# Performance work log

Hardware: AMD Instinct MI355X
Metric: run time of the kernel (lower is better)

Reference implementation:

```python
import jax, jax.numpy as jnp
import numpy as np

# MANO prior contact vertex indices (f1+f2+f3+f4+f5+f0 from CMap_loss3)
_F1 = [697,698,699,700,712,713,714,715,737,738,739,740,741,743,744,745,746,748,749,750,753,754,755,756,757,758,759,760,761,762,763,764,765,766,767,768]
_F2 = [46,47,48,49,164,165,166,167,194,195,223,237,238,280,281,298,301,317,320,323,324,325,326,327,328,329,330,331,332,333,340,341,342,343,344,345,346,347,348,349,350,351,352,353,354,355]
_F3 = [356,357,358,359,375,376,386,387,396,397,402,403,413,429,433,434,435,436,437,438,439,440,441,442,443,444,452,453,454,455,456,459,460,461,462,463,464,465,466,467]
_F4 = [468,469,470,471,484,485,486,496,497,506,507,513,514,524,545,546,547,548,549,550,551,552,553,555,563,564,565,566,567,570,572,573,574,575,576,577,578]
_F5 = [580,581,582,583,600,601,602,614,615,624,625,630,631,641,663,664,665,666,667,668,670,672,680,681,682,683,684,686,687,688,689,690,691,692,693,694,695]
_F0 = [73,96,98,99,772,774,775,777]
PRIOR_IDX = np.array(_F1 + _F2 + _F3 + _F4 + _F5 + _F0, dtype=np.int32)


def _sqdist(a, b):
    # a: [B,N,3], b: [B,M,3] -> squared distances [B,N,M] via ||a||^2+||b||^2-2ab
    a2 = jnp.sum(a * a, -1)          # [B,N]
    b2 = jnp.sum(b * b, -1)          # [B,M]
    ab = jnp.einsum('bnd,bmd->bnm', a, b)
    return jnp.maximum(a2[:, :, None] + b2[:, None, :] - 2.0 * ab, 0.0)


def _knn1(src, trg):
    # nearest neighbor (K=1): squared dists + indices, like pytorch3d knn_points
    d2 = _sqdist(src, trg)           # [B,N,M]
    return jnp.min(d2, -1), jnp.argmin(d2, -1)


def _verts_normals(verts, faces):
    # area-weighted vertex normals (pytorch3d verts_normals_packed)
    v0 = verts[:, faces[:, 0]]       # [B,F,3]
    v1 = verts[:, faces[:, 1]]
    v2 = verts[:, faces[:, 2]]
    fn = jnp.cross(v1 - v0, v2 - v0)
    vn = jnp.zeros_like(verts)
    vn = vn.at[:, faces[:, 0]].add(fn).at[:, faces[:, 1]].add(fn).at[:, faces[:, 2]].add(fn)
    return vn / (jnp.linalg.norm(vn, axis=-1, keepdims=True) + 1e-12)


def setup_inputs() -> dict:
    key = jax.random.key(0)
    ks = jax.random.split(key, 8)
    B, N1, V, F, Z, P = 64, 8192, 778, 1538, 64, 61
    scale = 0.1  # keep points in a 0.1 box so contact thresholds (0.005/0.01) fire
    return {
        'obj_xyz': jax.random.uniform(ks[0], (B, N1, 3), jnp.float32) * scale,
        'recon_xyz': jax.random.uniform(ks[1], (B, V, 3), jnp.float32) * scale,
        'gt_xyz': jax.random.uniform(ks[2], (B, V, 3), jnp.float32) * scale,
        'mean': jax.random.normal(ks[3], (B, Z), jnp.float32),
        'log_var': jax.random.normal(ks[4], (B, Z), jnp.float32),
        'recon_param': jax.random.normal(ks[5], (B, P), jnp.float32),
        'x_param': jax.random.normal(ks[6], (B, P), jnp.float32),
        'faces': jax.random.randint(ks[7], (F, 3), 0, V, jnp.int32),
    }


def reference(obj_xyz, recon_xyz, gt_xyz, mean, log_var, recon_param, x_param, faces):
    B = obj_xyz.shape[0]
    fB = jnp.float32(B)

    # KNN from object points to gt / reconstructed hand (squared dists)
    d_gt, _ = _knn1(obj_xyz, gt_xyz)            # [B,N1]
    d_rec, idx_rec = _knn1(obj_xyz, recon_xyz)  # [B,N1], [B,N1]

    # param loss: MSE sum / B
    param_loss = jnp.sum((recon_param - x_param) ** 2) / fB

    # CVAE loss: chamfer (point_reduction='sum', batch_reduction='mean') + KLD
    d2 = _sqdist(recon_xyz, gt_xyz)             # [B,778,778]
    recon_loss = jnp.mean(jnp.sum(jnp.min(d2, -1), -1)) + jnp.mean(jnp.sum(jnp.min(d2, -2), -1))
    KLD = -0.5 * jnp.sum(1.0 + log_var - mean ** 2 - jnp.exp(log_var)) / fB * 10.0
    cvae_loss = recon_loss + KLD

    # CMap_loss3: obj NN distance to prior hand contact verts, masked by cmap
    cmap = d_rec < 0.01 ** 2                    # [B,N1] bool
    prior = recon_xyz[:, PRIOR_IDX, :]          # [B,222,3]
    obj_CD, _ = _knn1(obj_xyz, prior)           # [B,N1]
    n_points = jnp.sum(cmap).astype(jnp.float32)
    cmap_loss = 3000.0 * jnp.sum(jnp.where(cmap, obj_CD, 0.0)) / (fB * n_points)

    # CMap consistency: contact-map overlap ratio
    recon_cmap = jnp.sqrt(d_rec) < 0.005
    gt_cmap = jnp.sqrt(d_gt) < 0.005
    gt_cnum = jnp.sum(gt_cmap).astype(jnp.float32) + 0.0001
    consistency_loss = -5.0 * jnp.sum(recon_cmap & gt_cmap).astype(jnp.float32) / gt_cnum

    # inter-penetration: gather NN hand verts/normals, sign of dot, masked dist sum
    vn = _verts_normals(recon_xyz, faces)                               # [B,778,3]
    nn_v = jnp.take_along_axis(recon_xyz, idx_rec[..., None], axis=1)   # [B,N1,3]
    nn_n = jnp.take_along_axis(vn, idx_rec[..., None], axis=1)          # [B,N1,3]
    interior = jnp.sum((nn_v - obj_xyz) * nn_n, -1) > 0                 # [B,N1]
    penetr_loss = 100.0 * jnp.sum(jnp.where(interior, d_rec, 0.0)) / fB

    a, b, c, d, e = 1.0, 0.1, 1000.0, 10.0, 10.0
    loss = a * cvae_loss + b * param_loss + c * cmap_loss + d * consistency_loss + e * penetr_loss
    return loss
```

## Files before the change

### kernel.cpp

```cpp
#include <hip/hip_runtime.h>
#include <math.h>

#define NB     64
#define N1V    8192
#define NPTS   (NB * N1V)
#define NV     778
#define NVP    780
#define NQ     195
#define SEG1Q  51
#define NFACE  1538
#define NZ     64
#define NPAR   61
#define NPRIOR 204
#define PPT    8
#define BIAS   0.0625f

#define REC_BLOCKS 256
#define GT_BLOCKS  256
#define CH_BLOCKS  128
#define NROLE_BLOCKS (REC_BLOCKS + GT_BLOCKS + CH_BLOCKS)
#define CMB_BLOCKS 64

#define BATCH_F4 2352
#define ACC_OFF (NB * BATCH_F4 * 4)
#define RC_OFF  (ACC_OFF + 16)
#define GC_OFF  (RC_OFF + NPTS / 32)

__device__ __constant__ int c_prior[NPRIOR] = {
  697,698,699,700,712,713,714,715,737,738,739,740,741,743,744,745,746,748,749,750,
  753,754,755,756,757,758,759,760,761,762,763,764,765,766,767,768,
  46,47,48,49,164,165,166,167,194,195,223,237,238,280,281,298,301,317,320,323,
  324,325,326,327,328,329,330,331,332,333,340,341,342,343,344,345,346,347,348,349,
  350,351,352,353,354,355,
  356,357,358,359,375,376,386,387,396,397,402,403,413,429,433,434,435,436,437,438,
  439,440,441,442,443,444,452,453,454,455,456,459,460,461,462,463,464,465,466,467,
  468,469,470,471,484,485,486,496,497,506,507,513,514,524,545,546,547,548,549,550,
  551,552,553,555,563,564,565,566,567,570,572,573,574,575,576,577,578,
  580,581,582,583,600,601,602,614,615,624,625,630,631,641,663,664,665,666,667,668,
  670,672,680,681,682,683,684,686,687,688,689,690,691,692,693,694,695,
  73,96,98,99,772,774,775,777
};

__global__ __launch_bounds__(256) void k_prep(const float* __restrict__ recon,
                                              const float* __restrict__ gt,
                                              const int* __restrict__ faces,
                                              float4* __restrict__ ws4,
                                              float* __restrict__ acc) {
    int b = blockIdx.x, tid = threadIdx.x;
    if (b == 0 && tid < 16) acc[tid] = 0.0f;
    __shared__ float4 s_r[NV];
    __shared__ float s_vnx[NV], s_vny[NV], s_vnz[NV];
    __shared__ unsigned int s_bm[25];
    __shared__ unsigned short s_pre[26];
    __shared__ unsigned short s_perm[NV];

    if (tid < 25) s_bm[tid] = 0u;
    __syncthreads();
    if (tid < NPRIOR) {
        int v = c_prior[tid];
        atomicOr(&s_bm[v >> 5], 1u << (v & 31));
    }
    const float* rb = recon + (size_t)b * NV * 3;
    const float* gb = gt    + (size_t)b * NV * 3;
    float4* gt4   = ws4 + (size_t)b * BATCH_F4;
    float4* rec4p = gt4 + NVP;
    float4* nrm4p = rec4p + NVP;
    for (int j = tid; j < NV; j += 256) {
        float x = rb[3*j], y = rb[3*j+1], z = rb[3*j+2];
        s_r[j] = make_float4(x, y, z, x*x + y*y + z*z + BIAS);
        x = gb[3*j]; y = gb[3*j+1]; z = gb[3*j+2];
        gt4[j] = make_float4(x, y, z, x*x + y*y + z*z);
        s_vnx[j] = 0.0f; s_vny[j] = 0.0f; s_vnz[j] = 0.0f;
    }
    if (tid < 2) gt4[NV + tid] = make_float4(0.f, 0.f, 0.f, 1e30f);
    __syncthreads();
    if (tid == 0) {
        unsigned int run = 0;
        for (int w = 0; w < 25; ++w) { s_pre[w] = (unsigned short)run; run += __popc(s_bm[w]); }
        s_pre[25] = (unsigned short)run;
    }
    __syncthreads();
    for (int j = tid; j < NV; j += 256) {
        int w = j >> 5;
        unsigned int below = s_bm[w] & ((1u << (j & 31)) - 1u);
        int rank = s_pre[w] + __popc(below);
        bool member = (s_bm[w] >> (j & 31)) & 1u;
        int pos = member ? rank : (NPRIOR + (j - rank));
        s_perm[pos] = (unsigned short)j;
    }
    for (int f = tid; f < NFACE; f += 256) {
        int i0 = faces[3*f], i1 = faces[3*f+1], i2 = faces[3*f+2];
        float4 p0 = s_r[i0], p1 = s_r[i1], p2 = s_r[i2];
        float e1x = p1.x - p0.x, e1y = p1.y - p0.y, e1z = p1.z - p0.z;
        float e2x = p2.x - p0.x, e2y = p2.y - p0.y, e2z = p2.z - p0.z;
        float fx = e1y * e2z - e1z * e2y;
        float fy = e1z * e2x - e1x * e2z;
        float fz = e1x * e2y - e1y * e2x;
        atomicAdd(&s_vnx[i0], fx); atomicAdd(&s_vny[i0], fy); atomicAdd(&s_vnz[i0], fz);
        atomicAdd(&s_vnx[i1], fx); atomicAdd(&s_vny[i1], fy); atomicAdd(&s_vnz[i1], fz);
        atomicAdd(&s_vnx[i2], fx); atomicAdd(&s_vny[i2], fy); atomicAdd(&s_vnz[i2], fz);
    }
    __syncthreads();
    for (int j = tid; j < NVP; j += 256) {
        if (j < NV) {
            int src = s_perm[j];
            rec4p[j] = s_r[src];
            float x = s_vnx[src], y = s_vny[src], z = s_vnz[src];
            float inv = 1.0f / (sqrtf(x*x + y*y + z*z) + 1e-12f);
            nrm4p[j] = make_float4(x * inv, y * inv, z * inv, 0.0f);
        } else {
            rec4p[j] = make_float4(0.f, 0.f, 0.f, 1e30f);
            nrm4p[j] = make_float4(0.f, 0.f, 1.f, 0.0f);
        }
    }
}

#define LOAD_PTS(ob)                                                          \
    const float4* ob4 = (const float4*)((ob) + (size_t)tid * 24);             \
    float4 q0 = ob4[0], q1 = ob4[1], q2 = ob4[2],                             \
           q3 = ob4[3], q4 = ob4[4], q5 = ob4[5];                             \
    float px[PPT], py[PPT], pz[PPT];                                          \
    px[0]=q0.x; py[0]=q0.y; pz[0]=q0.z;  px[1]=q0.w; py[1]=q1.x; pz[1]=q1.y;  \
    px[2]=q1.z; py[2]=q1.w; pz[2]=q2.x;  px[3]=q2.y; py[3]=q2.z; pz[3]=q2.w;  \
    px[4]=q3.x; py[4]=q3.y; pz[4]=q3.z;  px[5]=q3.w; py[5]=q4.x; pz[5]=q4.y;  \
    px[6]=q4.z; py[6]=q4.w; pz[6]=q5.x;  px[7]=q5.y; py[7]=q5.z; pz[7]=q5.w;

__global__ __launch_bounds__(256) void k_fused(const float* __restrict__ obj,
                                               const float4* __restrict__ ws4,
                                               float* __restrict__ acc,
                                               unsigned char* __restrict__ rcA,
                                               unsigned char* __restrict__ gcA) {
    __shared__ float4 s_t[NVP];
    __shared__ float s_red[3];
    int tid = threadIdx.x;
    int blk = blockIdx.x;

    if (blk < REC_BLOCKS) {
        int b = blk >> 2, chunk = blk & 3;
        const float4* base = ws4 + (size_t)b * BATCH_F4;
        const float4* rec4p = base + NVP;
        const float4* nrm4p = base + 2 * NVP;
        for (int j = tid; j < NVP; j += 256) s_t[j] = rec4p[j];
        if (tid < 3) s_red[tid] = 0.0f;
        __syncthreads();

        const float* ob = obj + ((size_t)b * N1V + (size_t)chunk * 2048) * 3;
        LOAD_PTS(ob)
        float nax[PPT], nay[PPT], naz[PPT], m[PPT];
        int q[PPT];
#pragma unroll
        for (int i = 0; i < PPT; ++i) {
            nax[i] = -2.0f * px[i]; nay[i] = -2.0f * py[i]; naz[i] = -2.0f * pz[i];
            m[i] = 3.4e38f; q[i] = 0;
        }
        float mp[PPT];
#pragma unroll 1
        for (int jq = 0; jq < SEG1Q; ++jq) {
            int j = 4 * jq;
            float4 t0 = s_t[j], t1 = s_t[j+1], t2 = s_t[j+2], t3 = s_t[j+3];
#pragma unroll
            for (int i = 0; i < PPT; ++i) {
                float d0 = fmaf(nax[i], t0.x, fmaf(nay[i], t0.y, fmaf(naz[i], t0.z, t0.w)));
                float d1 = fmaf(nax[i], t1.x, fmaf(nay[i], t1.y, fmaf(naz[i], t1.z, t1.w)));
                float d2 = fmaf(nax[i], t2.x, fmaf(nay[i], t2.y, fmaf(naz[i], t2.z, t2.w)));
                float d3 = fmaf(nax[i], t3.x, fmaf(nay[i], t3.y, fmaf(naz[i], t3.z, t3.w)));
                float mn = fminf(fminf(fminf(d0, d1), fminf(d2, d3)), m[i]);
                q[i] = (mn < m[i]) ? jq : q[i];
                m[i] = mn;
            }
        }
#pragma unroll
        for (int i = 0; i < PPT; ++i) mp[i] = m[i];
#pragma unroll 1
        for (int jq = SEG1Q; jq < NQ; ++jq) {
            int j = 4 * jq;
            float4 t0 = s_t[j], t1 = s_t[j+1], t2 = s_t[j+2], t3 = s_t[j+3];
#pragma unroll
            for (int i = 0; i < PPT; ++i) {
                float d0 = fmaf(nax[i], t0.x, fmaf(nay[i], t0.y, fmaf(naz[i], t0.z, t0.w)));
                float d1 = fmaf(nax[i], t1.x, fmaf(nay[i], t1.y, fmaf(naz[i], t1.z, t1.w)));
                float d2 = fmaf(nax[i], t2.x, fmaf(nay[i], t2.y, fmaf(naz[i], t2.z, t2.w)));
                float d3 = fmaf(nax[i], t3.x, fmaf(nay[i], t3.y, fmaf(naz[i], t3.z, t3.w)));
                float mn = fminf(fminf(fminf(d0, d1), fminf(d2, d3)), m[i]);
                q[i] = (mn < m[i]) ? jq : q[i];
                m[i] = mn;
            }
        }
        float lS_cmap = 0.0f, lN_cmap = 0.0f, lS_pen = 0.0f;
        unsigned int rcbits = 0;
#pragma unroll
        for (int i = 0; i < PPT; ++i) {
            float a2 = px[i]*px[i] + py[i]*py[i] + pz[i]*pz[i];
            float drec = fmaxf(a2 + (m[i]  - BIAS), 0.0f);
            float dpri = fmaxf(a2 + (mp[i] - BIAS), 0.0f);
            bool cm = drec < 1e-4f;
            bool rc = sqrtf(drec) < 0.005f;
            if (cm) { lS_cmap += dpri; lN_cmap += 1.0f; }
            if (rc) rcbits |= (1u << i);
            int jr = 4 * q[i];
            float4 t0 = s_t[jr], t1 = s_t[jr+1], t2 = s_t[jr+2], t3 = s_t[jr+3];
            float d0 = fmaf(nax[i], t0.x, fmaf(nay[i], t0.y, fmaf(naz[i], t0.z, t0.w)));
            float d1 = fmaf(nax[i], t1.x, fmaf(nay[i], t1.y, fmaf(naz[i], t1.z, t1.w)));
            float d2 = fmaf(nax[i], t2.x, fmaf(nay[i], t2.y, fmaf(naz[i], t2.z, t2.w)));
            float d3 = fmaf(nax[i], t3.x, fmaf(nay[i], t3.y, fmaf(naz[i], t3.z, t3.w)));
            float mmin = fminf(fminf(d0, d1), fminf(d2, d3));
            int off = (d0 == mmin) ? 0 : ((d1 == mmin) ? 1 : ((d2 == mmin) ? 2 : 3));
            int jstar = jr + off;
            float4 tS = s_t[jstar];
            float4 nr = nrm4p[jstar];
            float ddot = (tS.x - px[i]) * nr.x + (tS.y - py[i]) * nr.y
                       + (tS.z - pz[i]) * nr.z;
            if (ddot > 0.0f) lS_pen += drec;
        }
        rcA[(size_t)blk * 256 + tid] = (unsigned char)rcbits;
        atomicAdd(&s_red[0], lS_cmap);
        atomicAdd(&s_red[1], lN_cmap);
        atomicAdd(&s_red[2], lS_pen);
        __syncthreads();
        if (tid == 0) atomicAdd(&acc[3], s_red[0]);
        if (tid == 1) atomicAdd(&acc[4], s_red[1]);
        if (tid == 2) atomicAdd(&acc[7], s_red[2]);
        return;
    }

    if (blk < REC_BLOCKS + GT_BLOCKS) {
        int r = blk - REC_BLOCKS;
        int b = r >> 2, chunk = r & 3;
        const float4* gt4v = ws4 + (size_t)b * BATCH_F4;
        for (int j = tid; j < NVP; j += 256) s_t[j] = gt4v[j];
        if (tid == 0) s_red[0] = 0.0f;
        __syncthreads();

        const float* ob = obj + ((size_t)b * N1V + (size_t)chunk * 2048) * 3;
        LOAD_PTS(ob)
        float nax[PPT], nay[PPT], naz[PPT], mgt[PPT];
#pragma unroll
        for (int i = 0; i < PPT; ++i) {
            nax[i] = -2.0f * px[i]; nay[i] = -2.0f * py[i]; naz[i] = -2.0f * pz[i];
            mgt[i] = 3.4e38f;
        }
#pragma unroll 1
        for (int jq = 0; jq < NQ; ++jq) {
            int j = 4 * jq;
            float4 t0 = s_t[j], t1 = s_t[j+1], t2 = s_t[j+2], t3 = s_t[j+3];
#pragma unroll
            for (int i = 0; i < PPT; ++i) {
                float d0 = fmaf(nax[i], t0.x, fmaf(nay[i], t0.y, fmaf(naz[i], t0.z, t0.w)));
                float d1 = fmaf(nax[i], t1.x, fmaf(nay[i], t1.y, fmaf(naz[i], t1.z, t1.w)));
                float d2 = fmaf(nax[i], t2.x, fmaf(nay[i], t2.y, fmaf(naz[i], t2.z, t2.w)));
                float d3 = fmaf(nax[i], t3.x, fmaf(nay[i], t3.y, fmaf(naz[i], t3.z, t3.w)));
                mgt[i] = fminf(fminf(mgt[i], fminf(d0, d1)), fminf(d2, d3));
            }
        }
        float lN_gt = 0.0f;
        unsigned int gcbits = 0;
#pragma unroll
        for (int i = 0; i < PPT; ++i) {
            float a2 = px[i]*px[i] + py[i]*py[i] + pz[i]*pz[i];
            float dgt = fmaxf(a2 + mgt[i], 0.0f);
            if (sqrtf(dgt) < 0.005f) { lN_gt += 1.0f; gcbits |= (1u << i); }
        }
        gcA[(size_t)r * 256 + tid] = (unsigned char)gcbits;
        atomicAdd(&s_red[0], lN_gt);
        __syncthreads();
        if (tid == 0) atomicAdd(&acc[5], s_red[0]);
        return;
    }

    {
        int c   = blk - (REC_BLOCKS + GT_BLOCKS);
        int b   = c >> 1;
        int dir = c & 1;
        const float4* base = ws4 + (size_t)b * BATCH_F4;
        const float4* srcv = dir ? base : (base + NVP);
        const float4* tgtv = dir ? (base + NVP) : base;
        for (int j = tid; j < NVP; j += 256) s_t[j] = tgtv[j];
        if (tid == 0) s_red[0] = 0.0f;
        __syncthreads();

        const int CPT = 4;
        float nax[CPT], nay[CPT], naz[CPT], a2[CPT], m[CPT];
        bool valid[CPT];
#pragma unroll
        for (int k = 0; k < CPT; ++k) {
            int p = tid + 256 * k;
            valid[k] = (p < NV);
            float4 s = srcv[valid[k] ? p : 0];
            nax[k] = -2.0f * s.x; nay[k] = -2.0f * s.y; naz[k] = -2.0f * s.z;
            a2[k] = s.w;
            m[k] = 3.4e38f;
        }
#pragma unroll 1
        for (int j = 0; j < NVP; j += 4) {
            float4 t0 = s_t[j], t1 = s_t[j+1], t2 = s_t[j+2], t3 = s_t[j+3];
#pragma unroll
            for (int k = 0; k < CPT; ++k) {
                float d0 = fmaf(nax[k], t0.x, fmaf(nay[k], t0.y, fmaf(naz[k], t0.z, t0.w)));
                float d1 = fmaf(nax[k], t1.x, fmaf(nay[k], t1.y, fmaf(naz[k], t1.z, t1.w)));
                float d2 = fmaf(nax[k], t2.x, fmaf(nay[k], t2.y, fmaf(naz[k], t2.z, t2.w)));
                float d3 = fmaf(nax[k], t3.x, fmaf(nay[k], t3.y, fmaf(naz[k], t3.z, t3.w)));
                m[k] = fminf(fminf(m[k], fminf(d0, d1)), fminf(d2, d3));
            }
        }
        float local = 0.0f;
#pragma unroll
        for (int k = 0; k < CPT; ++k)
            if (valid[k]) local += fmaxf(a2[k] + m[k] - BIAS, 0.0f);
        atomicAdd(&s_red[0], local);
        __syncthreads();
        if (tid == 0) atomicAdd(&acc[2], s_red[0]);
    }
}

__global__ __launch_bounds__(256) void k_combine(float* __restrict__ acc,
                                                 const unsigned int* __restrict__ rcW,
                                                 const unsigned int* __restrict__ gcW,
                                                 const float* __restrict__ mean,
                                                 const float* __restrict__ log_var,
                                                 const float* __restrict__ rp,
                                                 const float* __restrict__ xp,
                                                 float* __restrict__ out) {
    int blk = blockIdx.x, tid = threadIdx.x;
    __shared__ float s_red[2];
    __shared__ unsigned int s_ticket;
    if (tid < 2) s_red[tid] = 0.0f;
    __syncthreads();
    int idx = blk * 256 + tid;
    unsigned int rc = rcW[idx], gc = gcW[idx];
    float cnt = (float)__popc(rc & gc);
    atomicAdd(&s_red[0], cnt);
    __syncthreads();
    if (tid == 0) atomicAdd(&acc[6], s_red[0]);
    __threadfence();
    if (tid == 0) s_ticket = atomicAdd((unsigned int*)&acc[15], 1u);
    __syncthreads();

    if (s_ticket == CMB_BLOCKS - 1) {
        if (tid < 2) s_red[tid] = 0.0f;
        __syncthreads();
        float s_param = 0.0f, s_kld = 0.0f;
        for (int i = tid; i < NB * NPAR; i += 256) {
            float d = rp[i] - xp[i];
            s_param += d * d;
        }
        for (int i = tid; i < NB * NZ; i += 256) {
            float m = mean[i], lv = log_var[i];
            s_kld += 1.0f + lv - m * m - expf(lv);
        }
        atomicAdd(&s_red[0], s_param);
        atomicAdd(&s_red[1], s_kld);
        __syncthreads();
        if (tid == 0) {
            const float fB = 64.0f;
            float a2v = atomicAdd(&acc[2], 0.0f);
            float a3  = atomicAdd(&acc[3], 0.0f);
            float a4  = atomicAdd(&acc[4], 0.0f);
            float a5  = atomicAdd(&acc[5], 0.0f);
            float a6  = atomicAdd(&acc[6], 0.0f);
            float a7  = atomicAdd(&acc[7], 0.0f);
            float param_loss  = s_red[0] / fB;
            float KLD         = -0.5f * s_red[1] / fB * 10.0f;
            float recon_loss  = a2v / fB;
            float cmap_loss   = 3000.0f * a3 / (fB * a4);
            float consistency = -5.0f * a6 / (a5 + 0.0001f);
            float penetr      = 100.0f * a7 / fB;
            out[0] = (recon_loss + KLD) + 0.1f * param_loss + 1000.0f * cmap_loss
                   + 10.0f * consistency + 10.0f * penetr;
        }
    }
}

extern "C" void kernel_launch(void* const* d_in, const int* in_sizes, int n_in,
                              void* d_out, int out_size, void* d_ws, size_t ws_size,
                              hipStream_t stream) {
    (void)in_sizes; (void)n_in; (void)out_size; (void)ws_size;
    const float* obj     = (const float*)d_in[0];
    const float* recon   = (const float*)d_in[1];
    const float* gt      = (const float*)d_in[2];
    const float* mean    = (const float*)d_in[3];
    const float* log_var = (const float*)d_in[4];
    const float* rp      = (const float*)d_in[5];
    const float* xp      = (const float*)d_in[6];
    const int*   faces   = (const int*)d_in[7];
    float* acc  = (float*)d_ws + ACC_OFF;
    float4* ws4 = (float4*)d_ws;
    unsigned char* rcA = (unsigned char*)((float*)d_ws + RC_OFF);
    unsigned char* gcA = (unsigned char*)((float*)d_ws + GC_OFF);
    float* out  = (float*)d_out;

    k_prep   <<<NB,           256, 0, stream>>>(recon, gt, faces, ws4, acc);
    k_fused  <<<NROLE_BLOCKS, 256, 0, stream>>>(obj, ws4, acc, rcA, gcA);
    k_combine<<<CMB_BLOCKS,   256, 0, stream>>>(acc, (const unsigned int*)rcA,
                                                (const unsigned int*)gcA,
                                                mean, log_var, rp, xp, out);
}
```

Baseline: 197.9 us.

## Stream hand vertices via scalar loads into SGPRs instead of LDS

```diff
diff --git a/kernel.cpp b/kernel.cpp
--- a/kernel.cpp
+++ b/kernel.cpp
@@ -26,7 +26,7 @@
 #define RC_OFF  (ACC_OFF + 16)
 #define GC_OFF  (RC_OFF + NPTS / 32)
 
-__device__ __constant__ int c_prior[NPRIOR] = {
+static constexpr int PRIOR_LIST[NPRIOR] = {
   697,698,699,700,712,713,714,715,737,738,739,740,741,743,744,745,746,748,749,750,
   753,754,755,756,757,758,759,760,761,762,763,764,765,766,767,768,
   46,47,48,49,164,165,166,167,194,195,223,237,238,280,281,298,301,317,320,323,
@@ -41,6 +41,20 @@
   73,96,98,99,772,774,775,777
 };
 
+struct PermT { unsigned short v[NV]; };
+static constexpr PermT make_perm() {
+    PermT t{};
+    bool mem[NV] = {};
+    for (int i = 0; i < NPRIOR; ++i) mem[PRIOR_LIST[i]] = true;
+    int a = 0, b = NPRIOR;
+    for (int j = 0; j < NV; ++j) {
+        if (mem[j]) t.v[a++] = (unsigned short)j;
+        else        t.v[b++] = (unsigned short)j;
+    }
+    return t;
+}
+__device__ __constant__ PermT c_perm = make_perm();
+
 __global__ __launch_bounds__(256) void k_prep(const float* __restrict__ recon,
                                               const float* __restrict__ gt,
                                               const int* __restrict__ faces,
@@ -50,16 +64,7 @@
     if (b == 0 && tid < 16) acc[tid] = 0.0f;
     __shared__ float4 s_r[NV];
     __shared__ float s_vnx[NV], s_vny[NV], s_vnz[NV];
-    __shared__ unsigned int s_bm[25];
-    __shared__ unsigned short s_pre[26];
-    __shared__ unsigned short s_perm[NV];
-
-    if (tid < 25) s_bm[tid] = 0u;
-    __syncthreads();
-    if (tid < NPRIOR) {
-        int v = c_prior[tid];
-        atomicOr(&s_bm[v >> 5], 1u << (v & 31));
-    }
+
     const float* rb = recon + (size_t)b * NV * 3;
     const float* gb = gt    + (size_t)b * NV * 3;
     float4* gt4   = ws4 + (size_t)b * BATCH_F4;
@@ -74,20 +79,6 @@
     }
     if (tid < 2) gt4[NV + tid] = make_float4(0.f, 0.f, 0.f, 1e30f);
     __syncthreads();
-    if (tid == 0) {
-        unsigned int run = 0;
-        for (int w = 0; w < 25; ++w) { s_pre[w] = (unsigned short)run; run += __popc(s_bm[w]); }
-        s_pre[25] = (unsigned short)run;
-    }
-    __syncthreads();
-    for (int j = tid; j < NV; j += 256) {
-        int w = j >> 5;
-        unsigned int below = s_bm[w] & ((1u << (j & 31)) - 1u);
-        int rank = s_pre[w] + __popc(below);
-        bool member = (s_bm[w] >> (j & 31)) & 1u;
-        int pos = member ? rank : (NPRIOR + (j - rank));
-        s_perm[pos] = (unsigned short)j;
-    }
     for (int f = tid; f < NFACE; f += 256) {
         int i0 = faces[3*f], i1 = faces[3*f+1], i2 = faces[3*f+2];
         float4 p0 = s_r[i0], p1 = s_r[i1], p2 = s_r[i2];
@@ -103,7 +94,7 @@
     __syncthreads();
     for (int j = tid; j < NVP; j += 256) {
         if (j < NV) {
-            int src = s_perm[j];
+            int src = c_perm.v[j];
             rec4p[j] = s_r[src];
             float x = s_vnx[src], y = s_vny[src], z = s_vnz[src];
             float inv = 1.0f / (sqrtf(x*x + y*y + z*z) + 1e-12f);
@@ -125,22 +116,72 @@
     px[4]=q3.x; py[4]=q3.y; pz[4]=q3.z;  px[5]=q3.w; py[5]=q4.x; pz[5]=q4.y;  \
     px[6]=q4.z; py[6]=q4.w; pz[6]=q5.x;  px[7]=q5.y; py[7]=q5.z; pz[7]=q5.w;
 
+__device__ __forceinline__ float min3f(float a, float b, float c) {
+    return fminf(fminf(a, b), c);
+}
+
+typedef float f4s __attribute__((ext_vector_type(4)));
+
+__device__ __forceinline__ f4s sld(unsigned long long base, unsigned int off) {
+    f4s r;
+    asm volatile("s_load_dwordx4 %0, %1, %2"
+                 : "=s"(r) : "s"(base), "s"(off));
+    return r;
+}
+#define SWAIT8(A0,A1,A2,A3,B0,B1,B2,B3)                                       \
+    asm volatile("s_waitcnt lgkmcnt(0)"                                       \
+                 : "+s"(A0),"+s"(A1),"+s"(A2),"+s"(A3),                       \
+                   "+s"(B0),"+s"(B1),"+s"(B2),"+s"(B3))
+#define SWAIT4(A0,A1,A2,A3)                                                   \
+    asm volatile("s_waitcnt lgkmcnt(0)"                                       \
+                 : "+s"(A0),"+s"(A1),"+s"(A2),"+s"(A3))
+
+#define QUAD_MINQ(T0,T1,T2,T3,JQ)                                             \
+    _Pragma("unroll")                                                         \
+    for (int i = 0; i < PPT; ++i) {                                           \
+        float d0 = fmaf(nax[i],(T0)[0], fmaf(nay[i],(T0)[1], fmaf(naz[i],(T0)[2],(T0)[3]))); \
+        float d1 = fmaf(nax[i],(T1)[0], fmaf(nay[i],(T1)[1], fmaf(naz[i],(T1)[2],(T1)[3]))); \
+        float d2 = fmaf(nax[i],(T2)[0], fmaf(nay[i],(T2)[1], fmaf(naz[i],(T2)[2],(T2)[3]))); \
+        float d3 = fmaf(nax[i],(T3)[0], fmaf(nay[i],(T3)[1], fmaf(naz[i],(T3)[2],(T3)[3]))); \
+        float u  = min3f(d0, d1, d2);                                         \
+        float mn = min3f(u, d3, m[i]);                                        \
+        q[i] = (mn < m[i]) ? (JQ) : q[i];                                     \
+        m[i] = mn;                                                            \
+    }
+
+#define QUAD_MIN(T0,T1,T2,T3)                                                 \
+    _Pragma("unroll")                                                         \
+    for (int i = 0; i < PPT; ++i) {                                           \
+        float d0 = fmaf(nax[i],(T0)[0], fmaf(nay[i],(T0)[1], fmaf(naz[i],(T0)[2],(T0)[3]))); \
+        float d1 = fmaf(nax[i],(T1)[0], fmaf(nay[i],(T1)[1], fmaf(naz[i],(T1)[2],(T1)[3]))); \
+        float d2 = fmaf(nax[i],(T2)[0], fmaf(nay[i],(T2)[1], fmaf(naz[i],(T2)[2],(T2)[3]))); \
+        float d3 = fmaf(nax[i],(T3)[0], fmaf(nay[i],(T3)[1], fmaf(naz[i],(T3)[2],(T3)[3]))); \
+        float u  = min3f(d0, d1, d2);                                         \
+        m[i] = min3f(u, d3, m[i]);                                            \
+    }
+
+#define LOAD_PAIR(BASE,OFF)                                                   \
+    f4s a0 = sld(BASE,(OFF)),      a1 = sld(BASE,(OFF)+16),                   \
+        a2 = sld(BASE,(OFF)+32),   a3 = sld(BASE,(OFF)+48);                   \
+    f4s b0 = sld(BASE,(OFF)+64),   b1 = sld(BASE,(OFF)+80),                   \
+        b2 = sld(BASE,(OFF)+96),   b3 = sld(BASE,(OFF)+112);                  \
+    SWAIT8(a0,a1,a2,a3,b0,b1,b2,b3);
+
 __global__ __launch_bounds__(256) void k_fused(const float* __restrict__ obj,
                                                const float4* __restrict__ ws4,
                                                float* __restrict__ acc,
                                                unsigned char* __restrict__ rcA,
                                                unsigned char* __restrict__ gcA) {
-    __shared__ float4 s_t[NVP];
     __shared__ float s_red[3];
     int tid = threadIdx.x;
     int blk = blockIdx.x;
 
     if (blk < REC_BLOCKS) {
         int b = blk >> 2, chunk = blk & 3;
-        const float4* base = ws4 + (size_t)b * BATCH_F4;
+        const float4* base  = ws4 + (size_t)b * BATCH_F4;
         const float4* rec4p = base + NVP;
         const float4* nrm4p = base + 2 * NVP;
-        for (int j = tid; j < NVP; j += 256) s_t[j] = rec4p[j];
+        unsigned long long recA = (unsigned long long)rec4p;
         if (tid < 3) s_red[tid] = 0.0f;
         __syncthreads();
 
@@ -155,50 +196,41 @@
         }
         float mp[PPT];
 #pragma unroll 1
-        for (int jq = 0; jq < SEG1Q; ++jq) {
-            int j = 4 * jq;
-            float4 t0 = s_t[j], t1 = s_t[j+1], t2 = s_t[j+2], t3 = s_t[j+3];
-#pragma unroll
-            for (int i = 0; i < PPT; ++i) {
-                float d0 = fmaf(nax[i], t0.x, fmaf(nay[i], t0.y, fmaf(naz[i], t0.z, t0.w)));
-                float d1 = fmaf(nax[i], t1.x, fmaf(nay[i], t1.y, fmaf(naz[i], t1.z, t1.w)));
-                float d2 = fmaf(nax[i], t2.x, fmaf(nay[i], t2.y, fmaf(naz[i], t2.z, t2.w)));
-                float d3 = fmaf(nax[i], t3.x, fmaf(nay[i], t3.y, fmaf(naz[i], t3.z, t3.w)));
-                float mn = fminf(fminf(fminf(d0, d1), fminf(d2, d3)), m[i]);
-                q[i] = (mn < m[i]) ? jq : q[i];
-                m[i] = mn;
-            }
+        for (int p = 0; p < 25; ++p) {
+            unsigned int off = (unsigned int)p * 128u;
+            LOAD_PAIR(recA, off)
+            QUAD_MINQ(a0,a1,a2,a3, 2*p)
+            QUAD_MINQ(b0,b1,b2,b3, 2*p+1)
+        }
+        {
+            unsigned int off = 50u * 64u;
+            f4s a0 = sld(recA,off), a1 = sld(recA,off+16),
+                a2 = sld(recA,off+32), a3 = sld(recA,off+48);
+            SWAIT4(a0,a1,a2,a3);
+            QUAD_MINQ(a0,a1,a2,a3, 50)
         }
 #pragma unroll
         for (int i = 0; i < PPT; ++i) mp[i] = m[i];
 #pragma unroll 1
-        for (int jq = SEG1Q; jq < NQ; ++jq) {
-            int j = 4 * jq;
-            float4 t0 = s_t[j], t1 = s_t[j+1], t2 = s_t[j+2], t3 = s_t[j+3];
-#pragma unroll
-            for (int i = 0; i < PPT; ++i) {
-                float d0 = fmaf(nax[i], t0.x, fmaf(nay[i], t0.y, fmaf(naz[i], t0.z, t0.w)));
-                float d1 = fmaf(nax[i], t1.x, fmaf(nay[i], t1.y, fmaf(naz[i], t1.z, t1.w)));
-                float d2 = fmaf(nax[i], t2.x, fmaf(nay[i], t2.y, fmaf(naz[i], t2.z, t2.w)));
-                float d3 = fmaf(nax[i], t3.x, fmaf(nay[i], t3.y, fmaf(naz[i], t3.z, t3.w)));
-                float mn = fminf(fminf(fminf(d0, d1), fminf(d2, d3)), m[i]);
-                q[i] = (mn < m[i]) ? jq : q[i];
-                m[i] = mn;
-            }
+        for (int p = 0; p < 72; ++p) {
+            unsigned int off = (51u + 2u*(unsigned int)p) * 64u;
+            LOAD_PAIR(recA, off)
+            QUAD_MINQ(a0,a1,a2,a3, 51 + 2*p)
+            QUAD_MINQ(b0,b1,b2,b3, 52 + 2*p)
         }
         float lS_cmap = 0.0f, lN_cmap = 0.0f, lS_pen = 0.0f;
         unsigned int rcbits = 0;
 #pragma unroll
         for (int i = 0; i < PPT; ++i) {
-            float a2 = px[i]*px[i] + py[i]*py[i] + pz[i]*pz[i];
-            float drec = fmaxf(a2 + (m[i]  - BIAS), 0.0f);
-            float dpri = fmaxf(a2 + (mp[i] - BIAS), 0.0f);
+            float a2v = px[i]*px[i] + py[i]*py[i] + pz[i]*pz[i];
+            float drec = fmaxf(a2v + (m[i]  - BIAS), 0.0f);
+            float dpri = fmaxf(a2v + (mp[i] - BIAS), 0.0f);
             bool cm = drec < 1e-4f;
             bool rc = sqrtf(drec) < 0.005f;
             if (cm) { lS_cmap += dpri; lN_cmap += 1.0f; }
             if (rc) rcbits |= (1u << i);
             int jr = 4 * q[i];
-            float4 t0 = s_t[jr], t1 = s_t[jr+1], t2 = s_t[jr+2], t3 = s_t[jr+3];
+            float4 t0 = rec4p[jr], t1 = rec4p[jr+1], t2 = rec4p[jr+2], t3 = rec4p[jr+3];
             float d0 = fmaf(nax[i], t0.x, fmaf(nay[i], t0.y, fmaf(naz[i], t0.z, t0.w)));
             float d1 = fmaf(nax[i], t1.x, fmaf(nay[i], t1.y, fmaf(naz[i], t1.z, t1.w)));
             float d2 = fmaf(nax[i], t2.x, fmaf(nay[i], t2.y, fmaf(naz[i], t2.z, t2.w)));
@@ -206,7 +238,7 @@
             float mmin = fminf(fminf(d0, d1), fminf(d2, d3));
             int off = (d0 == mmin) ? 0 : ((d1 == mmin) ? 1 : ((d2 == mmin) ? 2 : 3));
             int jstar = jr + off;
-            float4 tS = s_t[jstar];
+            float4 tS = rec4p[jstar];
             float4 nr = nrm4p[jstar];
             float ddot = (tS.x - px[i]) * nr.x + (tS.y - py[i]) * nr.y
                        + (tS.z - pz[i]) * nr.z;
@@ -226,38 +258,38 @@
     if (blk < REC_BLOCKS + GT_BLOCKS) {
         int r = blk - REC_BLOCKS;
         int b = r >> 2, chunk = r & 3;
-        const float4* gt4v = ws4 + (size_t)b * BATCH_F4;
-        for (int j = tid; j < NVP; j += 256) s_t[j] = gt4v[j];
+        unsigned long long gtA = (unsigned long long)(ws4 + (size_t)b * BATCH_F4);
         if (tid == 0) s_red[0] = 0.0f;
         __syncthreads();
 
         const float* ob = obj + ((size_t)b * N1V + (size_t)chunk * 2048) * 3;
         LOAD_PTS(ob)
-        float nax[PPT], nay[PPT], naz[PPT], mgt[PPT];
+        float nax[PPT], nay[PPT], naz[PPT], m[PPT];
 #pragma unroll
         for (int i = 0; i < PPT; ++i) {
             nax[i] = -2.0f * px[i]; nay[i] = -2.0f * py[i]; naz[i] = -2.0f * pz[i];
-            mgt[i] = 3.4e38f;
+            m[i] = 3.4e38f;
         }
 #pragma unroll 1
-        for (int jq = 0; jq < NQ; ++jq) {
-            int j = 4 * jq;
-            float4 t0 = s_t[j], t1 = s_t[j+1], t2 = s_t[j+2], t3 = s_t[j+3];
-#pragma unroll
-            for (int i = 0; i < PPT; ++i) {
-                float d0 = fmaf(nax[i], t0.x, fmaf(nay[i], t0.y, fmaf(naz[i], t0.z, t0.w)));
-                float d1 = fmaf(nax[i], t1.x, fmaf(nay[i], t1.y, fmaf(naz[i], t1.z, t1.w)));
-                float d2 = fmaf(nax[i], t2.x, fmaf(nay[i], t2.y, fmaf(naz[i], t2.z, t2.w)));
-                float d3 = fmaf(nax[i], t3.x, fmaf(nay[i], t3.y, fmaf(naz[i], t3.z, t3.w)));
-                mgt[i] = fminf(fminf(mgt[i], fminf(d0, d1)), fminf(d2, d3));
-            }
+        for (int p = 0; p < 97; ++p) {
+            unsigned int off = (unsigned int)p * 128u;
+            LOAD_PAIR(gtA, off)
+            QUAD_MIN(a0,a1,a2,a3)
+            QUAD_MIN(b0,b1,b2,b3)
+        }
+        {
+            unsigned int off = 194u * 64u;
+            f4s a0 = sld(gtA,off), a1 = sld(gtA,off+16),
+                a2 = sld(gtA,off+32), a3 = sld(gtA,off+48);
+            SWAIT4(a0,a1,a2,a3);
+            QUAD_MIN(a0,a1,a2,a3)
         }
         float lN_gt = 0.0f;
         unsigned int gcbits = 0;
 #pragma unroll
         for (int i = 0; i < PPT; ++i) {
-            float a2 = px[i]*px[i] + py[i]*py[i] + pz[i]*pz[i];
-            float dgt = fmaxf(a2 + mgt[i], 0.0f);
+            float a2v = px[i]*px[i] + py[i]*py[i] + pz[i]*pz[i];
+            float dgt = fmaxf(a2v + m[i], 0.0f);
             if (sqrtf(dgt) < 0.005f) { lN_gt += 1.0f; gcbits |= (1u << i); }
         }
         gcA[(size_t)r * 256 + tid] = (unsigned char)gcbits;
@@ -274,12 +306,12 @@
         const float4* base = ws4 + (size_t)b * BATCH_F4;
         const float4* srcv = dir ? base : (base + NVP);
         const float4* tgtv = dir ? (base + NVP) : base;
-        for (int j = tid; j < NVP; j += 256) s_t[j] = tgtv[j];
+        unsigned long long tgA = (unsigned long long)tgtv;
         if (tid == 0) s_red[0] = 0.0f;
         __syncthreads();
 
         const int CPT = 4;
-        float nax[CPT], nay[CPT], naz[CPT], a2[CPT], m[CPT];
+        float nax[CPT], nay[CPT], naz[CPT], sa2[CPT], m[CPT];
         bool valid[CPT];
 #pragma unroll
         for (int k = 0; k < CPT; ++k) {
@@ -287,25 +319,48 @@
             valid[k] = (p < NV);
             float4 s = srcv[valid[k] ? p : 0];
             nax[k] = -2.0f * s.x; nay[k] = -2.0f * s.y; naz[k] = -2.0f * s.z;
-            a2[k] = s.w;
+            sa2[k] = s.w;
             m[k] = 3.4e38f;
         }
 #pragma unroll 1
-        for (int j = 0; j < NVP; j += 4) {
-            float4 t0 = s_t[j], t1 = s_t[j+1], t2 = s_t[j+2], t3 = s_t[j+3];
+        for (int p = 0; p < 97; ++p) {
+            unsigned int off = (unsigned int)p * 128u;
+            LOAD_PAIR(tgA, off)
 #pragma unroll
             for (int k = 0; k < CPT; ++k) {
-                float d0 = fmaf(nax[k], t0.x, fmaf(nay[k], t0.y, fmaf(naz[k], t0.z, t0.w)));
-                float d1 = fmaf(nax[k], t1.x, fmaf(nay[k], t1.y, fmaf(naz[k], t1.z, t1.w)));
-                float d2 = fmaf(nax[k], t2.x, fmaf(nay[k], t2.y, fmaf(naz[k], t2.z, t2.w)));
-                float d3 = fmaf(nax[k], t3.x, fmaf(nay[k], t3.y, fmaf(naz[k], t3.z, t3.w)));
-                m[k] = fminf(fminf(m[k], fminf(d0, d1)), fminf(d2, d3));
+                float d0 = fmaf(nax[k],a0[0], fmaf(nay[k],a0[1], fmaf(naz[k],a0[2],a0[3])));
+                float d1 = fmaf(nax[k],a1[0], fmaf(nay[k],a1[1], fmaf(naz[k],a1[2],a1[3])));
+                float d2 = fmaf(nax[k],a2[0], fmaf(nay[k],a2[1], fmaf(naz[k],a2[2],a2[3])));
+                float d3 = fmaf(nax[k],a3[0], fmaf(nay[k],a3[1], fmaf(naz[k],a3[2],a3[3])));
+                float u = min3f(d0, d1, d2);
+                m[k] = min3f(u, d3, m[k]);
+                float e0 = fmaf(nax[k],b0[0], fmaf(nay[k],b0[1], fmaf(naz[k],b0[2],b0[3])));
+                float e1 = fmaf(nax[k],b1[0], fmaf(nay[k],b1[1], fmaf(naz[k],b1[2],b1[3])));
+                float e2 = fmaf(nax[k],b2[0], fmaf(nay[k],b2[1], fmaf(naz[k],b2[2],b2[3])));
+                float e3 = fmaf(nax[k],b3[0], fmaf(nay[k],b3[1], fmaf(naz[k],b3[2],b3[3])));
+                float v = min3f(e0, e1, e2);
+                m[k] = min3f(v, e3, m[k]);
             }
         }
+        {
+            unsigned int off = 194u * 64u;
+            f4s a0 = sld(tgA,off), a1 = sld(tgA,off+16),
+                a2 = sld(tgA,off+32), a3 = sld(tgA,off+48);
+            SWAIT4(a0,a1,a2,a3);
+#pragma unroll
+            for (int k = 0; k < CPT; ++k) {
+                float d0 = fmaf(nax[k],a0[0], fmaf(nay[k],a0[1], fmaf(naz[k],a0[2],a0[3])));
+                float d1 = fmaf(nax[k],a1[0], fmaf(nay[k],a1[1], fmaf(naz[k],a1[2],a1[3])));
+                float d2 = fmaf(nax[k],a2[0], fmaf(nay[k],a2[1], fmaf(naz[k],a2[2],a2[3])));
+                float d3 = fmaf(nax[k],a3[0], fmaf(nay[k],a3[1], fmaf(naz[k],a3[2],a3[3])));
+                float u = min3f(d0, d1, d2);
+                m[k] = min3f(u, d3, m[k]);
+            }
+        }
         float local = 0.0f;
 #pragma unroll
         for (int k = 0; k < CPT; ++k)
-            if (valid[k]) local += fmaxf(a2[k] + m[k] - BIAS, 0.0f);
+            if (valid[k]) local += fmaxf(sa2[k] + m[k] - BIAS, 0.0f);
         atomicAdd(&s_red[0], local);
         __syncthreads();
         if (tid == 0) atomicAdd(&acc[2], s_red[0]);
```

New measurement: 226.3 us. 14.3% more time.
